# Optimization experiments

Measured on AMD Instinct MI355X. Metric: run time of the kernel, lower is better.

The kernel has to match this reference:

```python
import jax, jax.numpy as jnp
import numpy as np

D_MODEL = 768
HEADS = 12
HEAD_DIM = D_MODEL // HEADS


def setup_inputs() -> dict:
    key = jax.random.key(0)
    ks = jax.random.split(key, 5)
    B, L = 4, 2048
    x = jax.random.normal(ks[0], (B, L, D_MODEL), dtype=jnp.float32)
    # torch nn.Linear init scale ~ 1/sqrt(fan_in); use small random weights
    s = 1.0 / np.sqrt(D_MODEL)
    W_qkv = jax.random.uniform(ks[1], (D_MODEL, 3 * D_MODEL), jnp.float32, -s, s)
    b_qkv = jax.random.uniform(ks[2], (3 * D_MODEL,), jnp.float32, -s, s)
    W_out = jax.random.uniform(ks[3], (D_MODEL, D_MODEL), jnp.float32, -s, s)
    b_out = jax.random.uniform(ks[4], (D_MODEL,), jnp.float32, -s, s)
    return {"x": x, "W_qkv": W_qkv, "b_qkv": b_qkv, "W_out": W_out, "b_out": b_out}


def reference(x, W_qkv, b_qkv, W_out, b_out):
    B, L, D = x.shape
    scale = jnp.sqrt(jnp.float32(HEAD_DIM))
    # qkv projection: [B, L, 3*D] -> [3, B, heads, L, head_dim]
    qkv = (x @ W_qkv + b_qkv).reshape(B, L, 3, HEADS, HEAD_DIM)
    qkv = jnp.transpose(qkv, (2, 0, 3, 1, 4))
    q, k, v = qkv[0], qkv[1], qkv[2]
    # full materialized attention, no mask
    scores = jnp.einsum("bhld,bhmd->bhlm", q, k) / scale  # [B, H, L, L]
    attn = jax.nn.softmax(scores, axis=-1)
    out = jnp.einsum("bhlm,bhmd->bhld", attn, v)  # [B, H, L, head_dim]
    out = jnp.transpose(out, (0, 2, 1, 3)).reshape(B, L, D)
    return out @ W_out + b_out
```

## Files before the change

kernel.cpp:

```cpp
#include <hip/hip_runtime.h>
#include <cmath>

typedef __bf16 bf16_t;
typedef __bf16 bf16x8 __attribute__((ext_vector_type(8)));
typedef __bf16 bf16x4 __attribute__((ext_vector_type(4)));
typedef float f32x4 __attribute__((ext_vector_type(4)));

#define MFMA(a, b, c) __builtin_amdgcn_mfma_f32_16x16x32_bf16((a), (b), (c), 0, 0, 0)
#define EXP2(x) __builtin_amdgcn_exp2f(x)

static constexpr int D = 768;
static constexpr int L = 2048;
static constexpr int NB = 4;
static constexpr int NH = 12;
static constexpr int HD = 64;
static constexpr int M = 8192;
static constexpr int NQKV = 2304;
#define QSCALE 0.18033688011112042f

__device__ __forceinline__ void glds16(const bf16_t* g, bf16_t* l) {
  __builtin_amdgcn_global_load_lds((const __attribute__((address_space(1))) void*)g,
                                   (__attribute__((address_space(3))) void*)l, 16, 0, 0);
}

__global__ __launch_bounds__(256) void cvt_bf16_kernel(const float* __restrict__ in,
                                                       bf16_t* __restrict__ out, int n8) {
  int g = blockIdx.x * 256 + threadIdx.x;
  if (g >= n8) return;
  const float4* p = (const float4*)in + (size_t)g * 2;
  float4 a = p[0], b = p[1];
  bf16x8 v = {(__bf16)a.x, (__bf16)a.y, (__bf16)a.z, (__bf16)a.w,
              (__bf16)b.x, (__bf16)b.y, (__bf16)b.z, (__bf16)b.w};
  *(bf16x8*)(out + (size_t)g * 8) = v;
}

__global__ __launch_bounds__(256) void transpose_cvt_kernel(const float* __restrict__ in,
                                                            bf16_t* __restrict__ out,
                                                            int rows, int cols) {
  __shared__ float t[32][33];
  int c0 = blockIdx.x * 32, r0 = blockIdx.y * 32;
  int tx = threadIdx.x, ty = threadIdx.y;
  for (int i = ty; i < 32; i += 8) t[i][tx] = in[(size_t)(r0 + i) * cols + c0 + tx];
  __syncthreads();
  for (int i = ty; i < 32; i += 8) out[(size_t)(c0 + i) * rows + r0 + tx] = (__bf16)t[tx][i];
}

__global__ __launch_bounds__(256) void gemm_qkv_kernel(const bf16_t* __restrict__ A,
                                                       const bf16_t* __restrict__ Bt,
                                                       const float* __restrict__ bias,
                                                       bf16_t* __restrict__ Qo,
                                                       bf16_t* __restrict__ Ko,
                                                       bf16_t* __restrict__ Vto) {
  __shared__ __align__(16) bf16_t As[2][128 * 32];
  __shared__ __align__(16) bf16_t Bs[2][128 * 32];
  const int tid = threadIdx.x;
  const int wave = tid >> 6, lane = tid & 63;
  const int quad = lane >> 4, l16 = lane & 15;
  const int wm = (wave >> 1) * 64, wn = (wave & 1) * 64;
  const int tm = blockIdx.x * 128, tn = blockIdx.y * 128;
  const int lr = tid >> 2, lc = (tid & 3) * 8;
  const bf16_t* Ag = A + (size_t)(tm + lr) * D + lc;
  const bf16_t* Bg = Bt + (size_t)(tn + lr) * D + lc;
  f32x4 acc[4][4] = {};
  for (int kt = 0; kt < D; kt += 64) {
    __syncthreads();
    glds16(Ag + kt, &As[0][wave * 512]);
    glds16(Ag + (size_t)64 * D + kt, &As[0][2048 + wave * 512]);
    glds16(Ag + kt + 32, &As[1][wave * 512]);
    glds16(Ag + (size_t)64 * D + kt + 32, &As[1][2048 + wave * 512]);
    glds16(Bg + kt, &Bs[0][wave * 512]);
    glds16(Bg + (size_t)64 * D + kt, &Bs[0][2048 + wave * 512]);
    glds16(Bg + kt + 32, &Bs[1][wave * 512]);
    glds16(Bg + (size_t)64 * D + kt + 32, &Bs[1][2048 + wave * 512]);
    __syncthreads();
#pragma unroll
    for (int kh = 0; kh < 2; kh++) {
      bf16x8 af[4], bfr[4];
#pragma unroll
      for (int i = 0; i < 4; i++)
        af[i] = *(const bf16x8*)&As[kh][(wm + i * 16 + l16) * 32 + quad * 8];
#pragma unroll
      for (int j = 0; j < 4; j++)
        bfr[j] = *(const bf16x8*)&Bs[kh][(wn + j * 16 + l16) * 32 + quad * 8];
#pragma unroll
      for (int i = 0; i < 4; i++)
#pragma unroll
        for (int j = 0; j < 4; j++) acc[i][j] = MFMA(af[i], bfr[j], acc[i][j]);
    }
  }
#pragma unroll
  for (int i = 0; i < 4; i++)
#pragma unroll
    for (int j = 0; j < 4; j++) {
      int n = tn + wn + j * 16 + l16;
      float bn = bias[n];
      int which = n / 768, rem = n - which * 768;
      int h = rem >> 6, d = rem & 63;
      int m0 = tm + wm + i * 16 + quad * 4;
      int b0 = m0 >> 11, l0 = m0 & 2047;
      int bh = b0 * NH + h;
      if (which == 2) {
        int blk = l0 >> 6;
        int v6 = l0 & 63;
        int t = v6 >> 5, w = v6 & 31;
        int lo = (w < 16);
        int q = (lo ? w : w - 16) >> 2;
        int p0 = t * 32 + q * 8 + (lo ? 0 : 4);
        bf16x4 wv;
#pragma unroll
        for (int r2 = 0; r2 < 4; r2++) wv[r2] = (__bf16)(acc[i][j][r2] + bn);
        *(bf16x4*)&Vto[(((size_t)bh * (L / 64) + blk) * HD + d) * 64 + p0] = wv;
      } else if (which == 0) {
#pragma unroll
        for (int r2 = 0; r2 < 4; r2++)
          Qo[((size_t)bh * L + l0 + r2) * HD + d] = (__bf16)((acc[i][j][r2] + bn) * QSCALE);
      } else {
#pragma unroll
        for (int r2 = 0; r2 < 4; r2++)
          Ko[((size_t)bh * L + l0 + r2) * HD + d] = (__bf16)(acc[i][j][r2] + bn);
      }
    }
}

__global__ __launch_bounds__(256) void attn_kernel(const bf16_t* __restrict__ Q,
                                                   const bf16_t* __restrict__ K,
                                                   const bf16_t* __restrict__ Vt,
                                                   bf16_t* __restrict__ O) {
  __shared__ __align__(16) bf16_t Ks[64][72];
  __shared__ __align__(16) bf16_t Vs[64][72];
  const int tid = threadIdx.x;
  const int wave = tid >> 6, lane = tid & 63;
  const int quad = lane >> 4, l16 = lane & 15;
  const int id = blockIdx.x;
  const int xcd = id & 7, slot = id >> 3;
  const int bh = xcd * 6 + (slot % 6);
  const int q0 = (slot / 6) * 128 + wave * 32;
  const bf16_t* Kb = K + (size_t)bh * L * HD;
  const bf16_t* Vb = Vt + (size_t)bh * HD * L;
  bf16x8 bq[2][2];
#pragma unroll
  for (int g = 0; g < 2; g++) {
    const bf16_t* Qp = Q + ((size_t)bh * L + q0 + g * 16 + l16) * HD + quad * 8;
    bq[g][0] = *(const bf16x8*)Qp;
    bq[g][1] = *(const bf16x8*)(Qp + 32);
  }
  f32x4 oacc[2][4] = {};
  float lacc[2] = {0.f, 0.f};
  const int st = tid >> 3, sc = (tid & 7) * 8;
  const bf16_t* pK0 = Kb + (size_t)st * HD + sc;
  const bf16_t* pK1 = Kb + (size_t)(st + 32) * HD + sc;
  const bf16_t* pV0 = Vb + (size_t)st * 64 + sc;
  const bf16_t* pV1 = Vb + (size_t)(st + 32) * 64 + sc;
  bf16x8 pk0 = *(const bf16x8*)pK0;
  bf16x8 pk1 = *(const bf16x8*)pK1;
  bf16x8 pv0 = *(const bf16x8*)pV0;
  bf16x8 pv1 = *(const bf16x8*)pV1;
  for (int j = 0; j < L / 64; j++) {
    __syncthreads();
    *(bf16x8*)&Ks[st][sc] = pk0;
    *(bf16x8*)&Ks[st + 32][sc] = pk1;
    *(bf16x8*)&Vs[st][sc] = pv0;
    *(bf16x8*)&Vs[st + 32][sc] = pv1;
    __syncthreads();
    if (j + 1 < L / 64) {
      pK0 += 64 * HD;
      pK1 += 64 * HD;
      pV0 += HD * 64;
      pV1 += HD * 64;
      pk0 = *(const bf16x8*)pK0;
      pk1 = *(const bf16x8*)pK1;
      pv0 = *(const bf16x8*)pV0;
      pv1 = *(const bf16x8*)pV1;
    }
    f32x4 s[2][4];
#pragma unroll
    for (int fn = 0; fn < 4; fn++) {
      bf16x8 ak0 = *(const bf16x8*)&Ks[fn * 16 + l16][quad * 8];
      bf16x8 ak1 = *(const bf16x8*)&Ks[fn * 16 + l16][32 + quad * 8];
#pragma unroll
      for (int g = 0; g < 2; g++) {
        f32x4 z = {};
        z = MFMA(ak0, bq[g][0], z);
        s[g][fn] = MFMA(ak1, bq[g][1], z);
      }
    }
    bf16x8 pq[2][2];
#pragma unroll
    for (int g = 0; g < 2; g++)
#pragma unroll
      for (int t = 0; t < 2; t++) {
        float e0 = EXP2(s[g][2 * t][0]), e1 = EXP2(s[g][2 * t][1]);
        float e2 = EXP2(s[g][2 * t][2]), e3 = EXP2(s[g][2 * t][3]);
        float e4 = EXP2(s[g][2 * t + 1][0]), e5 = EXP2(s[g][2 * t + 1][1]);
        float e6 = EXP2(s[g][2 * t + 1][2]), e7 = EXP2(s[g][2 * t + 1][3]);
        lacc[g] += ((e0 + e1) + (e2 + e3)) + ((e4 + e5) + (e6 + e7));
        bf16x8 w = {(__bf16)e0, (__bf16)e1, (__bf16)e2, (__bf16)e3,
                    (__bf16)e4, (__bf16)e5, (__bf16)e6, (__bf16)e7};
        pq[g][t] = w;
      }
#pragma unroll
    for (int fd = 0; fd < 4; fd++)
#pragma unroll
      for (int t = 0; t < 2; t++) {
        bf16x8 av = *(const bf16x8*)&Vs[fd * 16 + l16][t * 32 + quad * 8];
#pragma unroll
        for (int g = 0; g < 2; g++) oacc[g][fd] = MFMA(av, pq[g][t], oacc[g][fd]);
      }
  }
  const int b = bh / NH, h = bh - b * NH;
#pragma unroll
  for (int g = 0; g < 2; g++) {
    float ls = lacc[g];
    ls += __shfl_xor(ls, 16, 64);
    ls += __shfl_xor(ls, 32, 64);
    float rinv = 1.f / ls;
    int row = q0 + g * 16 + l16;
    bf16_t* Op = O + ((size_t)(b * L + row)) * D + h * HD;
#pragma unroll
    for (int fd = 0; fd < 4; fd++) {
      bf16x4 w;
#pragma unroll
      for (int r = 0; r < 4; r++) w[r] = (__bf16)(oacc[g][fd][r] * rinv);
      *(bf16x4*)(Op + fd * 16 + quad * 4) = w;
    }
  }
}

__global__ __launch_bounds__(256) void gemm_out_kernel(const bf16_t* __restrict__ A,
                                                       const bf16_t* __restrict__ Bt,
                                                       const float* __restrict__ bias,
                                                       float* __restrict__ Cg) {
  __shared__ __align__(16) bf16_t As[128 * 32];
  __shared__ __align__(16) bf16_t Bs[64 * 32];
  const int tid = threadIdx.x;
  const int wave = tid >> 6, lane = tid & 63;
  const int quad = lane >> 4, l16 = lane & 15;
  const int wm = (wave >> 1) * 64, wn = (wave & 1) * 32;
  const int tm = blockIdx.x * 128, tn = blockIdx.y * 64;
  const int lr = tid >> 2, lc = (tid & 3) * 8;
  const bf16_t* Ag = A + (size_t)(tm + lr) * D + lc;
  const bf16_t* Bg = Bt + (size_t)(tn + (lr & 63)) * D + lc;
  bf16_t* lA0 = &As[wave * 512];
  bf16_t* lA1 = &As[2048 + wave * 512];
  bf16_t* lB0 = &Bs[wave * 512];
  f32x4 acc[4][2] = {};
  for (int kt = 0; kt < D; kt += 32) {
    __syncthreads();
    glds16(Ag + kt, lA0);
    glds16(Ag + (size_t)64 * D + kt, lA1);
    glds16(Bg + kt, lB0);
    __syncthreads();
    bf16x8 af[4], bfr[2];
#pragma unroll
    for (int i = 0; i < 4; i++) af[i] = *(const bf16x8*)&As[(wm + i * 16 + l16) * 32 + quad * 8];
#pragma unroll
    for (int j = 0; j < 2; j++) bfr[j] = *(const bf16x8*)&Bs[(wn + j * 16 + l16) * 32 + quad * 8];
#pragma unroll
    for (int i = 0; i < 4; i++)
#pragma unroll
      for (int j = 0; j < 2; j++) acc[i][j] = MFMA(af[i], bfr[j], acc[i][j]);
  }
#pragma unroll
  for (int i = 0; i < 4; i++)
#pragma unroll
    for (int j = 0; j < 2; j++) {
      int n = tn + wn + j * 16 + l16;
      float bn = bias[n];
#pragma unroll
      for (int r2 = 0; r2 < 4; r2++) {
        int m = tm + wm + i * 16 + quad * 4 + r2;
        Cg[(size_t)m * D + n] = acc[i][j][r2] + bn;
      }
    }
}

extern "C" void kernel_launch(void* const* d_in, const int* in_sizes, int n_in,
                              void* d_out, int out_size, void* d_ws, size_t ws_size,
                              hipStream_t stream) {
  const float* x = (const float*)d_in[0];
  const float* Wqkv = (const float*)d_in[1];
  const float* bqkv = (const float*)d_in[2];
  const float* Wout = (const float*)d_in[3];
  const float* bout = (const float*)d_in[4];
  float* out = (float*)d_out;

  bf16_t* xb = (bf16_t*)d_ws;
  bf16_t* wqT = xb + (size_t)M * D;
  bf16_t* woT = wqT + (size_t)NQKV * D;
  bf16_t* Qb = woT + (size_t)D * D;
  bf16_t* Kb = Qb + (size_t)M * D;
  bf16_t* Vtb = Kb + (size_t)M * D;
  bf16_t* Ob = Vtb + (size_t)M * D;

  cvt_bf16_kernel<<<(M * D / 8 + 255) / 256, 256, 0, stream>>>(x, xb, M * D / 8);
  transpose_cvt_kernel<<<dim3(NQKV / 32, D / 32), dim3(32, 8), 0, stream>>>(Wqkv, wqT, D, NQKV);
  transpose_cvt_kernel<<<dim3(D / 32, D / 32), dim3(32, 8), 0, stream>>>(Wout, woT, D, D);
  gemm_qkv_kernel<<<dim3(M / 128, NQKV / 128), 256, 0, stream>>>(xb, wqT, bqkv, Qb, Kb, Vtb);
  attn_kernel<<<768, 256, 0, stream>>>(Qb, Kb, Vtb, Ob);
  gemm_out_kernel<<<dim3(M / 128, D / 64), 256, 0, stream>>>(Ob, woT, bout, out);
}
```

Baseline: 231.5 us.

## Merge weight transposes, shrink QKV GEMM K-step, vectorize Q/K epilogue stores

```diff
diff --git a/kernel.cpp b/kernel.cpp
--- a/kernel.cpp
+++ b/kernel.cpp
@@ -34,11 +34,17 @@
   *(bf16x8*)(out + (size_t)g * 8) = v;
 }
 
-__global__ __launch_bounds__(256) void transpose_cvt_kernel(const float* __restrict__ in,
-                                                            bf16_t* __restrict__ out,
-                                                            int rows, int cols) {
+__global__ __launch_bounds__(256) void transpose2_cvt_kernel(const float* __restrict__ w1,
+                                                             bf16_t* __restrict__ o1,
+                                                             const float* __restrict__ w2,
+                                                             bf16_t* __restrict__ o2) {
   __shared__ float t[32][33];
-  int c0 = blockIdx.x * 32, r0 = blockIdx.y * 32;
+  const bool second = blockIdx.x >= 72;
+  const float* in = second ? w2 : w1;
+  bf16_t* out = second ? o2 : o1;
+  const int cols = second ? 768 : 2304;
+  const int rows = 768;
+  int c0 = (second ? blockIdx.x - 72 : blockIdx.x) * 32, r0 = blockIdx.y * 32;
   int tx = threadIdx.x, ty = threadIdx.y;
   for (int i = ty; i < 32; i += 8) t[i][tx] = in[(size_t)(r0 + i) * cols + c0 + tx];
   __syncthreads();
@@ -51,55 +57,58 @@
                                                        bf16_t* __restrict__ Qo,
                                                        bf16_t* __restrict__ Ko,
                                                        bf16_t* __restrict__ Vto) {
-  __shared__ __align__(16) bf16_t As[2][128 * 32];
-  __shared__ __align__(16) bf16_t Bs[2][128 * 32];
+  __shared__ __align__(16) bf16_t As[128 * 32];
+  __shared__ __align__(16) bf16_t Bs[128 * 32];
   const int tid = threadIdx.x;
   const int wave = tid >> 6, lane = tid & 63;
   const int quad = lane >> 4, l16 = lane & 15;
   const int wm = (wave >> 1) * 64, wn = (wave & 1) * 64;
   const int tm = blockIdx.x * 128, tn = blockIdx.y * 128;
+  const int sel = tn / 768;
   const int lr = tid >> 2, lc = (tid & 3) * 8;
   const bf16_t* Ag = A + (size_t)(tm + lr) * D + lc;
   const bf16_t* Bg = Bt + (size_t)(tn + lr) * D + lc;
+  bf16_t* lA0 = &As[wave * 512];
+  bf16_t* lA1 = &As[2048 + wave * 512];
+  bf16_t* lB0 = &Bs[wave * 512];
+  bf16_t* lB1 = &Bs[2048 + wave * 512];
   f32x4 acc[4][4] = {};
-  for (int kt = 0; kt < D; kt += 64) {
-    __syncthreads();
-    glds16(Ag + kt, &As[0][wave * 512]);
-    glds16(Ag + (size_t)64 * D + kt, &As[0][2048 + wave * 512]);
-    glds16(Ag + kt + 32, &As[1][wave * 512]);
-    glds16(Ag + (size_t)64 * D + kt + 32, &As[1][2048 + wave * 512]);
-    glds16(Bg + kt, &Bs[0][wave * 512]);
-    glds16(Bg + (size_t)64 * D + kt, &Bs[0][2048 + wave * 512]);
-    glds16(Bg + kt + 32, &Bs[1][wave * 512]);
-    glds16(Bg + (size_t)64 * D + kt + 32, &Bs[1][2048 + wave * 512]);
-    __syncthreads();
-#pragma unroll
-    for (int kh = 0; kh < 2; kh++) {
-      bf16x8 af[4], bfr[4];
+  for (int kt = 0; kt < D; kt += 32) {
+    __syncthreads();
+    glds16(Ag + kt, lA0);
+    glds16(Ag + (size_t)64 * D + kt, lA1);
+    glds16(Bg + kt, lB0);
+    glds16(Bg + (size_t)64 * D + kt, lB1);
+    __syncthreads();
+    bf16x8 af[4], bfr[4];
+#pragma unroll
+    for (int i = 0; i < 4; i++) af[i] = *(const bf16x8*)&As[(wm + i * 16 + l16) * 32 + quad * 8];
+#pragma unroll
+    for (int j = 0; j < 4; j++) bfr[j] = *(const bf16x8*)&Bs[(wn + j * 16 + l16) * 32 + quad * 8];
+    if (sel == 2) {
 #pragma unroll
       for (int i = 0; i < 4; i++)
-        af[i] = *(const bf16x8*)&As[kh][(wm + i * 16 + l16) * 32 + quad * 8];
+#pragma unroll
+        for (int j = 0; j < 4; j++) acc[i][j] = MFMA(af[i], bfr[j], acc[i][j]);
+    } else {
 #pragma unroll
       for (int j = 0; j < 4; j++)
-        bfr[j] = *(const bf16x8*)&Bs[kh][(wn + j * 16 + l16) * 32 + quad * 8];
-#pragma unroll
-      for (int i = 0; i < 4; i++)
-#pragma unroll
-        for (int j = 0; j < 4; j++) acc[i][j] = MFMA(af[i], bfr[j], acc[i][j]);
-    }
-  }
-#pragma unroll
-  for (int i = 0; i < 4; i++)
-#pragma unroll
-    for (int j = 0; j < 4; j++) {
-      int n = tn + wn + j * 16 + l16;
-      float bn = bias[n];
-      int which = n / 768, rem = n - which * 768;
-      int h = rem >> 6, d = rem & 63;
-      int m0 = tm + wm + i * 16 + quad * 4;
-      int b0 = m0 >> 11, l0 = m0 & 2047;
-      int bh = b0 * NH + h;
-      if (which == 2) {
+#pragma unroll
+        for (int i = 0; i < 4; i++) acc[j][i] = MFMA(bfr[j], af[i], acc[j][i]);
+    }
+  }
+  if (sel == 2) {
+#pragma unroll
+    for (int i = 0; i < 4; i++)
+#pragma unroll
+      for (int j = 0; j < 4; j++) {
+        int n = tn + wn + j * 16 + l16;
+        float bn = bias[n];
+        int rem = n - 1536;
+        int h = rem >> 6, d = rem & 63;
+        int m0 = tm + wm + i * 16 + quad * 4;
+        int b0 = m0 >> 11, l0 = m0 & 2047;
+        int bh = b0 * NH + h;
         int blk = l0 >> 6;
         int v6 = l0 & 63;
         int t = v6 >> 5, w = v6 & 31;
@@ -110,16 +119,27 @@
 #pragma unroll
         for (int r2 = 0; r2 < 4; r2++) wv[r2] = (__bf16)(acc[i][j][r2] + bn);
         *(bf16x4*)&Vto[(((size_t)bh * (L / 64) + blk) * HD + d) * 64 + p0] = wv;
-      } else if (which == 0) {
-#pragma unroll
-        for (int r2 = 0; r2 < 4; r2++)
-          Qo[((size_t)bh * L + l0 + r2) * HD + d] = (__bf16)((acc[i][j][r2] + bn) * QSCALE);
-      } else {
-#pragma unroll
-        for (int r2 = 0; r2 < 4; r2++)
-          Ko[((size_t)bh * L + l0 + r2) * HD + d] = (__bf16)(acc[i][j][r2] + bn);
-      }
-    }
+      }
+  } else {
+    bf16_t* Out = sel ? Ko : Qo;
+    const float sc = sel ? 1.f : QSCALE;
+#pragma unroll
+    for (int j = 0; j < 4; j++) {
+      int nb = tn + wn + j * 16 + quad * 4;
+      float4 bj = *(const float4*)&bias[nb];
+      int rem = nb - sel * 768;
+      int h = rem >> 6, dlo = rem & 63;
+#pragma unroll
+      for (int i = 0; i < 4; i++) {
+        int m = tm + wm + i * 16 + l16;
+        int b0 = m >> 11, l = m & 2047;
+        bf16x4 w;
+#pragma unroll
+        for (int r2 = 0; r2 < 4; r2++) w[r2] = (__bf16)((acc[j][i][r2] + bj[r2]) * sc);
+        *(bf16x4*)&Out[((size_t)(b0 * NH + h) * L + l) * HD + dlo] = w;
+      }
+    }
+  }
 }
 
 __global__ __launch_bounds__(256) void attn_kernel(const bf16_t* __restrict__ Q,
@@ -293,8 +313,7 @@
   bf16_t* Ob = Vtb + (size_t)M * D;
 
   cvt_bf16_kernel<<<(M * D / 8 + 255) / 256, 256, 0, stream>>>(x, xb, M * D / 8);
-  transpose_cvt_kernel<<<dim3(NQKV / 32, D / 32), dim3(32, 8), 0, stream>>>(Wqkv, wqT, D, NQKV);
-  transpose_cvt_kernel<<<dim3(D / 32, D / 32), dim3(32, 8), 0, stream>>>(Wout, woT, D, D);
+  transpose2_cvt_kernel<<<dim3(96, 24), dim3(32, 8), 0, stream>>>(Wqkv, wqT, Wout, woT);
   gemm_qkv_kernel<<<dim3(M / 128, NQKV / 128), 256, 0, stream>>>(xb, wqT, bqkv, Qb, Kb, Vtb);
   attn_kernel<<<768, 256, 0, stream>>>(Qb, Kb, Vtb, Ob);
   gemm_out_kernel<<<dim3(M / 128, D / 64), 256, 0, stream>>>(Ob, woT, bout, out);
```

Measured after the change: 234.9 us. Within noise of the previous version (+1.5%).
